# Optimization experiments

Measured on AMD Instinct MI355X. Metric: run time of the kernel, lower is better.

The kernel has to match this reference:

```python
import jax, jax.numpy as jnp
import numpy as np

E, S, D, A, L, H, C = 8, 6000, 128, 16, 64, 256, 64
B = 50            # no_batches hardcoded in torch forward
T = S // B        # number of outer integration steps
DT = 0.5          # solver dt; t_horizon=[0,1] -> 2 reversible-Heun substeps
NSUB = 2
SQDT = float(np.sqrt(DT))


def setup_inputs():
    ks = jax.random.split(jax.random.key(0), 24)
    w = lambda k, shp, s=0.05: (jax.random.normal(k, shp) * s).astype(jnp.float32)
    z = lambda shp: jnp.zeros(shp, jnp.float32)
    return dict(
        xs=w(ks[0], (E, S, D), 1.0),
        actions=w(ks[1], (E, S, A), 1.0),
        z0_noise=w(ks[2], (T, E, B, L), 1.0),
        dW=w(ks[3], (T, NSUB, E * B, L), 1.0),
        enc_w1=w(ks[4], (E, D, H)), enc_b1=z((E, H)),
        enc_w2=w(ks[5], (E, H, C)), enc_b2=z((E, C)),
        qz0_w=w(ks[6], (E, C, 2 * L)), qz0_b=z((E, 2 * L)),
        act_w=w(ks[7], (E, L + A + D, L)), act_b=z((E, L)),
        fw1=w(ks[8], (L, H)), fb1=z((H,)),
        fw2=w(ks[9], (H, H)), fb2=z((H,)),
        fw3=w(ks[10], (H, L)), fb3=z((L,)),
        hw1=w(ks[11], (L, H)), hb1=z((H,)),
        hw2=w(ks[12], (H, H)), hb2=z((H,)),
        hw3=w(ks[13], (H, L)), hb3=z((L,)),
        gw1=w(ks[14], (L, H)), gb1=z((L, H)),
        gw2=w(ks[15], (L, H), 0.02), gb2=jnp.ones((L,), jnp.float32),
        pw1=w(ks[16], (E, L, H)), pb1=z((E, H)),
        pw2=w(ks[17], (E, H, H)), pb2=z((E, H)),
        pw3=w(ks[18], (E, H, D)), pb3=z((E, D)),
        pz0_mean=z((E, 1, L)), pz0_logstd=z((E, 1, L)),
    )


def reference(xs, actions, z0_noise, dW,
              enc_w1, enc_b1, enc_w2, enc_b2, qz0_w, qz0_b, act_w, act_b,
              fw1, fb1, fw2, fb2, fw3, fb3, hw1, hb1, hw2, hb2, hw3, hb3,
              gw1, gb1, gw2, gb2, pw1, pb1, pw2, pb2, pw3, pb3,
              pz0_mean, pz0_logstd):
    xs_r = xs.reshape(E, T, B, D).transpose(1, 0, 2, 3)       # [T,E,B,D]
    act_r = actions.reshape(E, T, B, A).transpose(1, 0, 2, 3)  # [T,E,B,A]

    def mlp3(y, w1, b1, w2, b2, w3, b3):
        h1 = jax.nn.sigmoid(y @ w1 + b1)
        h2 = jax.nn.sigmoid(h1 @ w2 + b2)
        return h2 @ w3 + b3

    def g_fn(y):  # per-latent-dim diagonal diffusion nets, vectorized over L
        hc = jax.nn.sigmoid(y[..., None] * gw1 + gb1)          # [N,L,H]
        return jnp.sum(hc * gw2, axis=-1) + gb2                # [N,L]

    def drift_all(zc):
        fz = mlp3(zc, fw1, fb1, fw2, fb2, fw3, fb3)
        hz = mlp3(zc, hw1, hb1, hw2, hb2, hw3, hb3)
        gz = g_fn(zc)
        u = (fz - hz) / gz
        return fz, gz, 0.5 * jnp.sum(u * u, axis=-1)           # logqp drift

    def sde_solve(zini, dWs):  # reversible Heun, Stratonovich, logqp-augmented
        zc = zh = zini
        lc = lh = jnp.zeros(zini.shape[0], zini.dtype)
        fz, gz, lf = drift_all(zc)
        for k in range(NSUB):
            dWk = dWs[k] * SQDT
            zh_n = 2.0 * zc - zh + fz * DT + gz * dWk
            lh_n = 2.0 * lc - lh + lf * DT
            fz1, gz1, lf1 = drift_all(zh_n)
            zc = zc + 0.5 * (fz + fz1) * DT + 0.5 * (gz + gz1) * dWk
            lc = lc + 0.5 * (lf + lf1) * DT
            zh, lh, fz, gz, lf = zh_n, lh_n, fz1, gz1, lf1
        return zc, lc

    def step(z_prev, inp):
        i, x_i, a_i, n_i, dW_i = inp
        c1 = jax.nn.sigmoid(jnp.einsum('ebd,edh->ebh', x_i, enc_w1) + enc_b1[:, None])
        ctx = jnp.einsum('ebh,ehc->ebc', c1, enc_w2) + enc_b2[:, None]
        q = jnp.einsum('ebc,eck->ebk', ctx, qz0_w) + qz0_b[:, None]
        qm, ql = q[..., :L], q[..., L:]
        z0 = qm + jnp.exp(ql) * n_i
        z_in = jnp.where(i == 0, z0, z_prev)
        lat = jnp.concatenate([z_in, a_i, x_i], axis=-1)
        z_enc = jnp.einsum('ebf,efl->ebl', lat, act_w) + act_b[:, None]
        zf, lr = sde_solve(z_enc.reshape(E * B, L), dW_i)
        z_new = zf.reshape(E, B, L)
        p1 = jax.nn.sigmoid(jnp.einsum('ebl,elh->ebh', z_new, pw1) + pb1[:, None])
        p2 = jax.nn.sigmoid(jnp.einsum('ebh,ehk->ebk', p1, pw2) + pb2[:, None])
        xm = jnp.einsum('ebh,ehd->ebd', p2, pw3) + pb3[:, None]
        # KL(q(z0) || p(z0)) elementwise, p has mean pz0_mean, logstd pz0_logstd
        kl = (pz0_logstd - ql
              + (jnp.exp(2.0 * ql) + (qm - pz0_mean) ** 2) / (2.0 * jnp.exp(2.0 * pz0_logstd))
              - 0.5)
        logqp0 = kl.sum(-1).mean(-1)  # [E]
        return z_new, (xm, lr.reshape(E, B), logqp0)

    z_init = jnp.zeros((E, B, L), xs.dtype)
    _, (xm_all, lr_all, lq0_all) = jax.lax.scan(
        step, z_init, (jnp.arange(T), xs_r, act_r, z0_noise, dW))
    predicted_xs = xm_all.transpose(1, 0, 2, 3).reshape(E, T * B, D)
    logqp_path = lr_all.mean(-1).sum(0) + lq0_all.sum(0)  # [E]
    return logqp_path, predicted_xs
```

## Files before the change

kernel.cpp:

```cpp
#include <hip/hip_runtime.h>
#include <math.h>

#define E 8
#define S 6000
#define D 128
#define A 16
#define L 64
#define H 256
#define C 64
#define B 50
#define T 120
#define NSUB 2
#define FLAT 208
#define RTOT 400
#define RPB 10
#define NBLK (RTOT / RPB)
#define BGRP 10
#define NBG 5

#define DT 0.5f
#define SQDT 0.70710678118654752440f

#define GNT 4096
#define GYMIN (-128.0f)
#define GDY 0.0625f
#define GINVDY 16.0f

typedef __attribute__((ext_vector_type(8))) short bf16x8;
typedef __attribute__((ext_vector_type(4))) float f32x4;

#define MFMA16(a, b, c) __builtin_amdgcn_mfma_f32_16x16x32_bf16(a, b, c, 0, 0, 0)

__device__ __forceinline__ float sigf(float x) { return 1.0f / (1.0f + __expf(-x)); }

__device__ __forceinline__ unsigned short f2bf(float x) {
    union { float f; unsigned u; } v; v.f = x;
    unsigned r = (v.u + 0x7FFFu + ((v.u >> 16) & 1u)) >> 16;
    return (unsigned short)r;
}

__global__ void gtab_kernel(const float* __restrict__ gw1, const float* __restrict__ gb1,
                            const float* __restrict__ gw2, const float* __restrict__ gb2,
                            float* __restrict__ tab) {
    int idx = blockIdx.x * blockDim.x + threadIdx.x;
    if (idx >= L * GNT) return;
    int l = idx / GNT, i = idx % GNT;
    float y = GYMIN + (float)i * GDY;
    const float* w1 = gw1 + l * H;
    const float* b1 = gb1 + l * H;
    const float* w2 = gw2 + l * H;
    float acc = gb2[l];
    #pragma unroll 4
    for (int h = 0; h < H; ++h) acc += w2[h] * sigf(y * w1[h] + b1[h]);
    tab[idx] = acc;
}

__global__ void packB_kernel(const float* __restrict__ src, unsigned short* __restrict__ dst,
                             int K, int N) {
    int idx = blockIdx.x * 256 + threadIdx.x;
    if (idx >= K * N) return;
    int j = idx & 7;
    int lane = (idx >> 3) & 63;
    int t2 = idx >> 9;
    int KC = K >> 5;
    int kc = t2 % KC, n = t2 / KC;
    int k = (kc << 5) + ((lane >> 4) << 3) + j;
    int c = (n << 4) + (lane & 15);
    dst[idx] = f2bf(src[k * N + c]);
}

__global__ void packAW_kernel(const float* __restrict__ aw, unsigned short* __restrict__ dst) {
    int idx = blockIdx.x * 256 + threadIdx.x;
    if (idx >= E * L * L) return;
    int e = idx >> 12;
    int rem = idx & 4095;
    int j = rem & 7;
    int lane = (rem >> 3) & 63;
    int t2 = rem >> 9;
    int kc = t2 & 1, n = t2 >> 1;
    int k = (kc << 5) + ((lane >> 4) << 3) + j;
    int c = (n << 4) + (lane & 15);
    dst[idx] = f2bf(aw[((size_t)e * FLAT + k) * L + c]);
}

__global__ __launch_bounds__(256) void enc_kernel(const float* __restrict__ xs, const float* __restrict__ z0n,
                           const float* __restrict__ ew1, const float* __restrict__ eb1,
                           const float* __restrict__ ew2, const float* __restrict__ eb2,
                           const float* __restrict__ qw,  const float* __restrict__ qb,
                           const float* __restrict__ pm,  const float* __restrict__ pl,
                           float* __restrict__ z0buf, float* __restrict__ logqp0p) {
    int bid = blockIdx.x;
    int bg = bid % NBG; int te = bid / NBG; int e = te % E; int t = te / E;
    int tid = threadIdx.x;
    __shared__ float xsh[BGRP][D];
    __shared__ float c1s[BGRP][H];
    __shared__ float part[4][C][BGRP];
    __shared__ float ctxs[BGRP][C];
    __shared__ float qs[BGRP][2 * L];

    for (int i = tid; i < BGRP * D; i += 256) {
        int j = i / D, d = i % D;
        xsh[j][d] = xs[((size_t)e * S + (size_t)t * B + bg * BGRP + j) * D + d];
    }
    __syncthreads();
    {
        float bias = eb1[e * H + tid];
        float acc[BGRP];
        #pragma unroll
        for (int j = 0; j < BGRP; ++j) acc[j] = bias;
        const float* w = ew1 + (size_t)e * D * H + tid;
        #pragma unroll 4
        for (int d = 0; d < D; ++d) {
            float wv = w[(size_t)d * H];
            #pragma unroll
            for (int j = 0; j < BGRP; ++j) acc[j] += xsh[j][d] * wv;
        }
        #pragma unroll
        for (int j = 0; j < BGRP; ++j) c1s[j][tid] = sigf(acc[j]);
    }
    __syncthreads();
    {
        int c = tid & 63, kq = tid >> 6;
        float acc[BGRP];
        #pragma unroll
        for (int j = 0; j < BGRP; ++j) acc[j] = 0.f;
        const float* w = ew2 + (size_t)e * H * C + c;
        #pragma unroll 4
        for (int h = kq * 64; h < kq * 64 + 64; ++h) {
            float wv = w[(size_t)h * C];
            #pragma unroll
            for (int j = 0; j < BGRP; ++j) acc[j] += c1s[j][h] * wv;
        }
        #pragma unroll
        for (int j = 0; j < BGRP; ++j) part[kq][c][j] = acc[j];
    }
    __syncthreads();
    if (tid < C) {
        float bias = eb2[e * C + tid];
        #pragma unroll
        for (int j = 0; j < BGRP; ++j)
            ctxs[j][tid] = part[0][tid][j] + part[1][tid][j] + part[2][tid][j] + part[3][tid][j] + bias;
    }
    __syncthreads();
    if (tid < 2 * L) {
        float bias = qb[e * 2 * L + tid];
        float acc[BGRP];
        #pragma unroll
        for (int j = 0; j < BGRP; ++j) acc[j] = bias;
        const float* w = qw + (size_t)e * C * 2 * L + tid;
        #pragma unroll 4
        for (int c = 0; c < C; ++c) {
            float wv = w[(size_t)c * 2 * L];
            #pragma unroll
            for (int j = 0; j < BGRP; ++j) acc[j] += ctxs[j][c] * wv;
        }
        #pragma unroll
        for (int j = 0; j < BGRP; ++j) qs[j][tid] = acc[j];
    }
    __syncthreads();
    if (tid < L) {
        int l = tid;
        float kacc = 0.f;
        float m = pm[e * L + l], ls = pl[e * L + l];
        float inv2e = 1.0f / (2.0f * __expf(2.0f * ls));
        #pragma unroll
        for (int j = 0; j < BGRP; ++j) {
            float qm = qs[j][l], ql = qs[j][L + l];
            if (t == 0) {
                int b = bg * BGRP + j;
                float n = z0n[((size_t)e * B + b) * L + l];
                z0buf[((size_t)e * B + b) * L + l] = qm + __expf(ql) * n;
            }
            float dq = qm - m;
            kacc += ls - ql + (__expf(2.f * ql) + dq * dq) * inv2e - 0.5f;
        }
        #pragma unroll
        for (int off = 32; off; off >>= 1) kacc += __shfl_xor(kacc, off);
        if (l == 0) logqp0p[bid] = kacc / (float)B;
    }
}

__global__ __launch_bounds__(64) void ax_kernel(const float* __restrict__ xs, const float* __restrict__ actions,
                          const float* __restrict__ aw, const float* __restrict__ ab,
                          float* __restrict__ ax) {
    int bid = blockIdx.x;
    int bg = bid % NBG; int te = bid / NBG; int e = te % E; int t = te / E;
    int tid = threadIdx.x;
    __shared__ float xrow[BGRP][D];
    __shared__ float arow[BGRP][A];
    for (int i = tid; i < BGRP * D; i += 64) {
        int j = i / D, d = i % D;
        xrow[j][d] = xs[((size_t)e * S + (size_t)t * B + bg * BGRP + j) * D + d];
    }
    for (int i = tid; i < BGRP * A; i += 64) {
        int j = i / A, a = i % A;
        arow[j][a] = actions[((size_t)e * S + (size_t)t * B + bg * BGRP + j) * A + a];
    }
    __syncthreads();
    int l = tid;
    float acc[BGRP];
    float bias = ab[e * L + l];
    #pragma unroll
    for (int j = 0; j < BGRP; ++j) acc[j] = bias;
    const float* awp = aw + ((size_t)e * FLAT + L) * L + l;
    #pragma unroll 4
    for (int a = 0; a < A; ++a) {
        float wv = awp[(size_t)a * L];
        #pragma unroll
        for (int j = 0; j < BGRP; ++j) acc[j] += arow[j][a] * wv;
    }
    const float* xwp = aw + ((size_t)e * FLAT + L + A) * L + l;
    #pragma unroll 4
    for (int d = 0; d < D; ++d) {
        float wv = xwp[(size_t)d * L];
        #pragma unroll
        for (int j = 0; j < BGRP; ++j) acc[j] += xrow[j][d] * wv;
    }
    size_t rbase = (size_t)t * RTOT + e * B + bg * BGRP;
    #pragma unroll
    for (int j = 0; j < BGRP; ++j) ax[(rbase + j) * L + l] = acc[j];
}

__global__ __launch_bounds__(512, 2) void seq_kernel(
    const unsigned short* __restrict__ pkAW, const float* __restrict__ dW,
    const float* __restrict__ z0buf, const float* __restrict__ axbuf,
    const unsigned short* __restrict__ pk1, const unsigned short* __restrict__ pk2,
    const unsigned short* __restrict__ pk3,
    const float* __restrict__ fb1, const float* __restrict__ hb1,
    const float* __restrict__ fb2, const float* __restrict__ hb2,
    const float* __restrict__ fb3, const float* __restrict__ hb3,
    const float* __restrict__ gtab, float* __restrict__ z_all, float* __restrict__ rowlr)
{
    __shared__ __align__(16) bf16x8 w1L[4096];
    __shared__ __align__(16) unsigned short ybf[16 * 64];
    __shared__ __align__(16) unsigned short o1[2][16 * 256];
    __shared__ __align__(16) unsigned short o2[2][16 * 256];
    __shared__ float zcS[16][64], zhA[16][64], zhB[16][64];
    __shared__ float fzb[2][16][64], gzb[2][16][64];
    __shared__ float lfb[2][16], lcS[16], lrsum[16];

    int tid = threadIdx.x;
    int wv = tid >> 6;
    int lane = tid & 63;
    int rA = lane & 15, kg = lane >> 4;
    int r_base = blockIdx.x * RPB;
    int e = blockIdx.x / 5;
    int sw = (rA & 7) << 3;

    for (int i = tid; i < 4096; i += 512) w1L[i] = ((const bf16x8*)pk1)[i];

    int net = wv >> 2;
    int nt0 = (wv & 3) << 2;
    int n0 = wv & 3;
    bf16x8 W0r[2], W2r[32], W3r[8];
    {
        const bf16x8* p0 = (const bf16x8*)pkAW + (e << 9);
        #pragma unroll
        for (int kc = 0; kc < 2; ++kc) W0r[kc] = p0[(n0 * 2 + kc) * 64 + lane];
        const bf16x8* p2 = (const bf16x8*)pk2 + net * 8192;
        #pragma unroll
        for (int i2 = 0; i2 < 4; ++i2)
            #pragma unroll
            for (int kc = 0; kc < 8; ++kc)
                W2r[i2 * 8 + kc] = p2[((nt0 + i2) * 8 + kc) * 64 + lane];
        const bf16x8* p3 = (const bf16x8*)pk3 + net * 2048;
        #pragma unroll
        for (int kc = 0; kc < 8; ++kc) W3r[kc] = p3[(n0 * 8 + kc) * 64 + lane];
    }
    float biasA[4], biasB[4], biasC;
    {
        const float* b1 = net ? hb1 : fb1;
        const float* b2 = net ? hb2 : fb2;
        const float* b3 = net ? hb3 : fb3;
        #pragma unroll
        for (int i2 = 0; i2 < 4; ++i2) {
            biasA[i2] = b1[((nt0 + i2) << 4) + rA];
            biasB[i2] = b2[((nt0 + i2) << 4) + rA];
        }
        biasC = b3[(n0 << 4) + rA];
    }

    for (int i = tid; i < RPB * L; i += 512) {
        int r = i >> 6;
        ybf[i ^ ((r & 7) << 3)] = f2bf(z0buf[(size_t)r_base * L + i]);
    }
    if (tid < 16) lrsum[tid] = 0.f;
    __syncthreads();

    float* fhp = (float*)o1;

    auto drift = [&](const float (*__restrict__ ysrc)[64], int bo) {
        {
            bf16x8 A0 = *(const bf16x8*)&ybf[((rA << 6) + (kg << 3)) ^ sw];
            bf16x8 A1 = *(const bf16x8*)&ybf[((rA << 6) + 32 + (kg << 3)) ^ sw];
            f32x4 acc[4];
            #pragma unroll
            for (int i2 = 0; i2 < 4; ++i2) {
                acc[i2] = (f32x4){biasA[i2], biasA[i2], biasA[i2], biasA[i2]};
                acc[i2] = MFMA16(A0, w1L[net * 2048 + ((nt0 + i2) * 2 + 0) * 64 + lane], acc[i2]);
                acc[i2] = MFMA16(A1, w1L[net * 2048 + ((nt0 + i2) * 2 + 1) * 64 + lane], acc[i2]);
            }
            unsigned short* o1n = o1[net];
            #pragma unroll
            for (int i2 = 0; i2 < 4; ++i2) {
                int c = ((nt0 + i2) << 4) + rA;
                #pragma unroll
                for (int rr = 0; rr < 4; ++rr) {
                    int r = (kg << 2) + rr;
                    o1n[((r << 8) + c) ^ ((r & 7) << 3)] = f2bf(sigf(acc[i2][rr]));
                }
            }
        }
        __syncthreads();
        {
            const unsigned short* o1n = o1[net];
            f32x4 acc[4];
            #pragma unroll
            for (int i2 = 0; i2 < 4; ++i2)
                acc[i2] = (f32x4){biasB[i2], biasB[i2], biasB[i2], biasB[i2]};
            #pragma unroll
            for (int kc = 0; kc < 8; ++kc) {
                bf16x8 Ak = *(const bf16x8*)&o1n[((rA << 8) + (kc << 5) + (kg << 3)) ^ sw];
                #pragma unroll
                for (int i2 = 0; i2 < 4; ++i2)
                    acc[i2] = MFMA16(Ak, W2r[i2 * 8 + kc], acc[i2]);
            }
            unsigned short* o2n = o2[net];
            #pragma unroll
            for (int i2 = 0; i2 < 4; ++i2) {
                int c = ((nt0 + i2) << 4) + rA;
                #pragma unroll
                for (int rr = 0; rr < 4; ++rr) {
                    int r = (kg << 2) + rr;
                    o2n[((r << 8) + c) ^ ((r & 7) << 3)] = f2bf(sigf(acc[i2][rr]));
                }
            }
        }
        __syncthreads();
        {
            const unsigned short* o2n = o2[net];
            f32x4 acc = (f32x4){biasC, biasC, biasC, biasC};
            #pragma unroll
            for (int kc = 0; kc < 8; ++kc) {
                bf16x8 Ak = *(const bf16x8*)&o2n[((rA << 8) + (kc << 5) + (kg << 3)) ^ sw];
                acc = MFMA16(Ak, W3r[kc], acc);
            }
            int c = (n0 << 4) + rA;
            #pragma unroll
            for (int rr = 0; rr < 4; ++rr)
                fhp[net * 1024 + (((kg << 2) + rr) << 6) + c] = acc[rr];
        }
        __syncthreads();
        #pragma unroll
        for (int pass = 0; pass < 2; ++pass) {
            int r = wv + (pass << 3);
            if (r < RPB) {
                int l = lane;
                float fv = fhp[(r << 6) + l];
                float hv = fhp[1024 + (r << 6) + l];
                float yl = ysrc[r][l];
                float x = (yl - GYMIN) * GINVDY;
                x = fminf(fmaxf(x, 0.0f), (float)(GNT - 2) + 0.999f);
                int ii = (int)x;
                float fr = x - (float)ii;
                const float* tl = gtab + ((size_t)l << 12);
                float gv = tl[ii] * (1.0f - fr) + tl[ii + 1] * fr;
                float u = (fv - hv) / gv;
                fzb[bo][r][l] = fv;
                gzb[bo][r][l] = gv;
                float us = u * u;
                #pragma unroll
                for (int off = 32; off; off >>= 1) us += __shfl_xor(us, off);
                if (l == 0) lfb[bo][r] = 0.5f * us;
            }
        }
        __syncthreads();
    };

    for (int t = 0; t < T; ++t) {
        size_t axb = ((size_t)t * RTOT + r_base) * L;
        size_t db0 = ((size_t)(t * 2 + 0) * RTOT + r_base) * L;
        size_t db1 = ((size_t)(t * 2 + 1) * RTOT + r_base) * L;
        float ax0 = axbuf[axb + tid];
        float dwA0 = dW[db0 + tid] * SQDT;
        float dwB0 = dW[db1 + tid] * SQDT;
        float ax1 = 0.f, dwA1 = 0.f, dwB1 = 0.f;
        if (tid < RPB * L - 512) {
            ax1  = axbuf[axb + 512 + tid];
            dwA1 = dW[db0 + 512 + tid] * SQDT;
            dwB1 = dW[db1 + 512 + tid] * SQDT;
        }
        if (wv < 4) {
            bf16x8 Z0 = *(const bf16x8*)&ybf[((rA << 6) + (kg << 3)) ^ sw];
            bf16x8 Z1 = *(const bf16x8*)&ybf[((rA << 6) + 32 + (kg << 3)) ^ sw];
            f32x4 acc = (f32x4){0.f, 0.f, 0.f, 0.f};
            acc = MFMA16(Z0, W0r[0], acc);
            acc = MFMA16(Z1, W0r[1], acc);
            int c = (n0 << 4) + rA;
            #pragma unroll
            for (int rr = 0; rr < 4; ++rr)
                zcS[(kg << 2) + rr][c] = acc[rr];
        }
        if (tid < 16) lcS[tid] = 0.f;
        __syncthreads();
        {
            int r = tid >> 6, l = tid & 63;
            float v = zcS[r][l] + ax0;
            zcS[r][l] = v; zhA[r][l] = v;
            ybf[tid ^ ((r & 7) << 3)] = f2bf(v);
            if (tid < RPB * L - 512) {
                int i2 = tid + 512, r2 = i2 >> 6, l2 = i2 & 63;
                float v2 = zcS[r2][l2] + ax1;
                zcS[r2][l2] = v2; zhA[r2][l2] = v2;
                ybf[i2 ^ ((r2 & 7) << 3)] = f2bf(v2);
            }
        }
        __syncthreads();

        drift(zcS, 0);

        float (*zh)[64] = zhA;
        float (*zt)[64] = zhB;
        int cur = 0;
        #pragma unroll
        for (int k2 = 0; k2 < NSUB; ++k2) {
            int nxt = cur ^ 1;
            float dwv0 = k2 ? dwB0 : dwA0;
            float dwv1 = k2 ? dwB1 : dwA1;
            {
                int r = tid >> 6, l = tid & 63;
                float v = 2.f * zcS[r][l] - zh[r][l] + fzb[cur][r][l] * DT + gzb[cur][r][l] * dwv0;
                zt[r][l] = v;
                ybf[tid ^ ((r & 7) << 3)] = f2bf(v);
                if (tid < RPB * L - 512) {
                    int i2 = tid + 512, r2 = i2 >> 6, l2 = i2 & 63;
                    float v2 = 2.f * zcS[r2][l2] - zh[r2][l2] + fzb[cur][r2][l2] * DT + gzb[cur][r2][l2] * dwv1;
                    zt[r2][l2] = v2;
                    ybf[i2 ^ ((r2 & 7) << 3)] = f2bf(v2);
                }
            }
            __syncthreads();
            drift(zt, nxt);
            {
                int r = tid >> 6, l = tid & 63;
                zcS[r][l] += 0.5f * (fzb[cur][r][l] + fzb[nxt][r][l]) * DT
                           + 0.5f * (gzb[cur][r][l] + gzb[nxt][r][l]) * dwv0;
                if (tid < RPB * L - 512) {
                    int i2 = tid + 512, r2 = i2 >> 6, l2 = i2 & 63;
                    zcS[r2][l2] += 0.5f * (fzb[cur][r2][l2] + fzb[nxt][r2][l2]) * DT
                                 + 0.5f * (gzb[cur][r2][l2] + gzb[nxt][r2][l2]) * dwv1;
                }
            }
            if (tid < RPB) lcS[tid] += 0.5f * (lfb[cur][tid] + lfb[nxt][tid]) * DT;
            { float (*tmp)[64] = zh; zh = zt; zt = tmp; }
            cur = nxt;
            __syncthreads();
        }
        {
            int r = tid >> 6;
            float v = zcS[r][tid & 63];
            z_all[((size_t)t * RTOT + r_base) * L + tid] = v;
            ybf[tid ^ ((r & 7) << 3)] = f2bf(v);
            if (tid < RPB * L - 512) {
                int i2 = tid + 512, r2 = i2 >> 6;
                float v2 = zcS[r2][i2 & 63];
                z_all[((size_t)t * RTOT + r_base) * L + i2] = v2;
                ybf[i2 ^ ((r2 & 7) << 3)] = f2bf(v2);
            }
        }
        if (tid < RPB) lrsum[tid] += lcS[tid];
        __syncthreads();
    }
    if (tid < RPB) rowlr[r_base + tid] = lrsum[tid];
}

__global__ __launch_bounds__(256) void proj_kernel(const float* __restrict__ z_all,
                            const float* __restrict__ pw1, const float* __restrict__ pb1,
                            const float* __restrict__ pw2, const float* __restrict__ pb2,
                            const float* __restrict__ pw3, const float* __restrict__ pb3,
                            float* __restrict__ out) {
    int bid = blockIdx.x;
    int bg = bid % NBG; int te = bid / NBG; int e = te % E; int t = te / E;
    int tid = threadIdx.x;
    __shared__ float zs[BGRP][L];
    __shared__ float p1s[BGRP][H];
    __shared__ float p2s[BGRP][H];
    __shared__ float part3[D][BGRP];
    size_t rbase = (size_t)t * RTOT + e * B + bg * BGRP;
    for (int i = tid; i < BGRP * L; i += 256) {
        int j = i >> 6, ll = i & 63;
        zs[j][ll] = z_all[(rbase + j) * L + ll];
    }
    __syncthreads();
    {
        float bias = pb1[e * H + tid];
        float acc[BGRP];
        #pragma unroll
        for (int j = 0; j < BGRP; ++j) acc[j] = bias;
        const float* w = pw1 + (size_t)e * L * H + tid;
        #pragma unroll 4
        for (int k = 0; k < L; ++k) {
            float wv = w[(size_t)k * H];
            #pragma unroll
            for (int j = 0; j < BGRP; ++j) acc[j] += zs[j][k] * wv;
        }
        #pragma unroll
        for (int j = 0; j < BGRP; ++j) p1s[j][tid] = sigf(acc[j]);
    }
    __syncthreads();
    {
        float bias = pb2[e * H + tid];
        float acc[BGRP];
        #pragma unroll
        for (int j = 0; j < BGRP; ++j) acc[j] = bias;
        const float* w = pw2 + (size_t)e * H * H + tid;
        #pragma unroll 4
        for (int k = 0; k < H; ++k) {
            float wv = w[(size_t)k * H];
            #pragma unroll
            for (int j = 0; j < BGRP; ++j) acc[j] += p1s[j][k] * wv;
        }
        #pragma unroll
        for (int j = 0; j < BGRP; ++j) p2s[j][tid] = sigf(acc[j]);
    }
    __syncthreads();
    float acc3[BGRP];
    {
        int dd = tid & 127, kh = tid >> 7;
        #pragma unroll
        for (int j = 0; j < BGRP; ++j) acc3[j] = 0.f;
        const float* w = pw3 + (size_t)e * H * D + dd;
        #pragma unroll 4
        for (int k = kh * 128; k < kh * 128 + 128; ++k) {
            float wv = w[(size_t)k * D];
            #pragma unroll
            for (int j = 0; j < BGRP; ++j) acc3[j] += p2s[j][k] * wv;
        }
        if (kh == 1) {
            #pragma unroll
            for (int j = 0; j < BGRP; ++j) part3[dd][j] = acc3[j];
        }
    }
    __syncthreads();
    if (tid < D) {
        float bias = pb3[e * D + tid];
        #pragma unroll
        for (int j = 0; j < BGRP; ++j) {
            out[8 + ((size_t)e * S + (size_t)t * B + bg * BGRP + j) * D + tid]
                = acc3[j] + part3[tid][j] + bias;
        }
    }
}

__global__ void fin_kernel(const float* __restrict__ logqp0p, const float* __restrict__ rowlr,
                           float* __restrict__ out) {
    int e = threadIdx.x;
    if (e < E) {
        float acc = 0.f;
        for (int t = 0; t < T; ++t)
            for (int bg = 0; bg < NBG; ++bg)
                acc += logqp0p[(t * E + e) * NBG + bg];
        float s = 0.f;
        for (int b = 0; b < B; ++b) s += rowlr[e * B + b];
        out[e] = acc + s / (float)B;
    }
}

extern "C" void kernel_launch(void* const* d_in, const int* in_sizes, int n_in,
                              void* d_out, int out_size, void* d_ws, size_t ws_size,
                              hipStream_t stream) {
    const float* xs      = (const float*)d_in[0];
    const float* actions = (const float*)d_in[1];
    const float* z0n     = (const float*)d_in[2];
    const float* dWp     = (const float*)d_in[3];
    const float* ew1     = (const float*)d_in[4];
    const float* eb1     = (const float*)d_in[5];
    const float* ew2     = (const float*)d_in[6];
    const float* eb2     = (const float*)d_in[7];
    const float* qw      = (const float*)d_in[8];
    const float* qb      = (const float*)d_in[9];
    const float* aw      = (const float*)d_in[10];
    const float* ab      = (const float*)d_in[11];
    const float* fw1     = (const float*)d_in[12];
    const float* fb1     = (const float*)d_in[13];
    const float* fw2     = (const float*)d_in[14];
    const float* fb2     = (const float*)d_in[15];
    const float* fw3     = (const float*)d_in[16];
    const float* fb3     = (const float*)d_in[17];
    const float* hw1     = (const float*)d_in[18];
    const float* hb1     = (const float*)d_in[19];
    const float* hw2     = (const float*)d_in[20];
    const float* hb2     = (const float*)d_in[21];
    const float* hw3     = (const float*)d_in[22];
    const float* hb3     = (const float*)d_in[23];
    const float* gw1     = (const float*)d_in[24];
    const float* gb1     = (const float*)d_in[25];
    const float* gw2     = (const float*)d_in[26];
    const float* gb2     = (const float*)d_in[27];
    const float* pw1     = (const float*)d_in[28];
    const float* pb1     = (const float*)d_in[29];
    const float* pw2     = (const float*)d_in[30];
    const float* pb2     = (const float*)d_in[31];
    const float* pw3     = (const float*)d_in[32];
    const float* pb3     = (const float*)d_in[33];
    const float* pm      = (const float*)d_in[34];
    const float* pl      = (const float*)d_in[35];

    float* ws      = (float*)d_ws;
    float* z0buf   = ws;
    float* axbuf   = z0buf + 25600;
    float* z_all   = axbuf + 3072000;
    float* logqp0p = z_all + 3072000;
    float* rowlr   = logqp0p + 4800;
    float* gtab    = rowlr + 400;
    unsigned short* pku = (unsigned short*)(gtab + 262144);
    unsigned short* pk1 = pku;
    unsigned short* pk2 = pk1 + 32768;
    unsigned short* pk3 = pk2 + 131072;
    unsigned short* pkAW = pk3 + 32768;
    float* out     = (float*)d_out;

    packB_kernel<<<64,  256, 0, stream>>>(fw1, pk1,          64, 256);
    packB_kernel<<<64,  256, 0, stream>>>(hw1, pk1 + 16384,  64, 256);
    packB_kernel<<<256, 256, 0, stream>>>(fw2, pk2,          256, 256);
    packB_kernel<<<256, 256, 0, stream>>>(hw2, pk2 + 65536,  256, 256);
    packB_kernel<<<64,  256, 0, stream>>>(fw3, pk3,          256, 64);
    packB_kernel<<<64,  256, 0, stream>>>(hw3, pk3 + 16384,  256, 64);
    packAW_kernel<<<128, 256, 0, stream>>>(aw, pkAW);
    gtab_kernel<<<1024, 256, 0, stream>>>(gw1, gb1, gw2, gb2, gtab);
    enc_kernel<<<T * E * NBG, 256, 0, stream>>>(xs, z0n, ew1, eb1, ew2, eb2, qw, qb, pm, pl, z0buf, logqp0p);
    ax_kernel<<<T * E * NBG, 64, 0, stream>>>(xs, actions, aw, ab, axbuf);
    seq_kernel<<<NBLK, 512, 0, stream>>>(pkAW, dWp, z0buf, axbuf,
                                         pk1, pk2, pk3,
                                         fb1, hb1, fb2, hb2, fb3, hb3,
                                         gtab, z_all, rowlr);
    proj_kernel<<<T * E * NBG, 256, 0, stream>>>(z_all, pw1, pb1, pw2, pb2, pw3, pb3, out);
    fin_kernel<<<1, 64, 0, stream>>>(logqp0p, rowlr, out);
}
```

Before: 3.155 ms.

## Double seq_kernel threads to 1024 and split MLP work across more waves

The sequential SDE kernel now launches 1024 threads per block instead of 512. Each wave handles half as many output tiles in layers 1 and 2, and layer 3 is split along K into two halves whose partial sums are added through shared memory. The diffusion-table lookup is also moved earlier, into the z-update phase, so its global loads overlap the MLP. The aim is to shorten the serial critical path of each step. The cost is more waves contending at every barrier and an extra shared-memory reduction.

```diff
diff --git a/kernel.cpp b/kernel.cpp
--- a/kernel.cpp
+++ b/kernel.cpp
@@ -221,7 +221,7 @@
     for (int j = 0; j < BGRP; ++j) ax[(rbase + j) * L + l] = acc[j];
 }
 
-__global__ __launch_bounds__(512, 2) void seq_kernel(
+__global__ __launch_bounds__(1024, 4) void seq_kernel(
     const unsigned short* __restrict__ pkAW, const float* __restrict__ dW,
     const float* __restrict__ z0buf, const float* __restrict__ axbuf,
     const unsigned short* __restrict__ pk1, const unsigned short* __restrict__ pk2,
@@ -235,75 +235,89 @@
     __shared__ __align__(16) unsigned short ybf[16 * 64];
     __shared__ __align__(16) unsigned short o1[2][16 * 256];
     __shared__ __align__(16) unsigned short o2[2][16 * 256];
+    __shared__ float fh2[2][2][RPB][64];
     __shared__ float zcS[16][64], zhA[16][64], zhB[16][64];
-    __shared__ float fzb[2][16][64], gzb[2][16][64];
-    __shared__ float lfb[2][16], lcS[16], lrsum[16];
+    __shared__ float fzb[2][RPB][64], gzb[2][RPB][64];
+    __shared__ float lfb[2][RPB], lcS[RPB], lrsum[RPB];
 
     int tid = threadIdx.x;
     int wv = tid >> 6;
     int lane = tid & 63;
     int rA = lane & 15, kg = lane >> 4;
+    int sw = (rA & 7) << 3;
     int r_base = blockIdx.x * RPB;
     int e = blockIdx.x / 5;
-    int sw = (rA & 7) << 3;
-
-    for (int i = tid; i < 4096; i += 512) w1L[i] = ((const bf16x8*)pk1)[i];
-
-    int net = wv >> 2;
-    int nt0 = (wv & 3) << 2;
+
+    for (int i = tid; i < 4096; i += 1024) w1L[i] = ((const bf16x8*)pk1)[i];
+
+    int net = wv >> 3;
+    int na = (wv & 7) << 1;
+    int cnet = wv >> 3, crem = wv & 7, n0c = crem >> 1, kh = crem & 1;
     int n0 = wv & 3;
-    bf16x8 W0r[2], W2r[32], W3r[8];
+
+    bf16x8 W0r[2], W2r[16], W3r[4];
     {
         const bf16x8* p0 = (const bf16x8*)pkAW + (e << 9);
-        #pragma unroll
-        for (int kc = 0; kc < 2; ++kc) W0r[kc] = p0[(n0 * 2 + kc) * 64 + lane];
+        W0r[0] = p0[(n0 * 2 + 0) * 64 + lane];
+        W0r[1] = p0[(n0 * 2 + 1) * 64 + lane];
         const bf16x8* p2 = (const bf16x8*)pk2 + net * 8192;
         #pragma unroll
-        for (int i2 = 0; i2 < 4; ++i2)
+        for (int i2 = 0; i2 < 2; ++i2)
             #pragma unroll
             for (int kc = 0; kc < 8; ++kc)
-                W2r[i2 * 8 + kc] = p2[((nt0 + i2) * 8 + kc) * 64 + lane];
-        const bf16x8* p3 = (const bf16x8*)pk3 + net * 2048;
-        #pragma unroll
-        for (int kc = 0; kc < 8; ++kc) W3r[kc] = p3[(n0 * 8 + kc) * 64 + lane];
-    }
-    float biasA[4], biasB[4], biasC;
+                W2r[i2 * 8 + kc] = p2[((na + i2) * 8 + kc) * 64 + lane];
+        const bf16x8* p3 = (const bf16x8*)pk3 + cnet * 2048;
+        #pragma unroll
+        for (int kc = 0; kc < 4; ++kc)
+            W3r[kc] = p3[(n0c * 8 + kh * 4 + kc) * 64 + lane];
+    }
+    float biasA[2], biasB[2], biasC;
     {
         const float* b1 = net ? hb1 : fb1;
         const float* b2 = net ? hb2 : fb2;
-        const float* b3 = net ? hb3 : fb3;
-        #pragma unroll
-        for (int i2 = 0; i2 < 4; ++i2) {
-            biasA[i2] = b1[((nt0 + i2) << 4) + rA];
-            biasB[i2] = b2[((nt0 + i2) << 4) + rA];
-        }
-        biasC = b3[(n0 << 4) + rA];
-    }
-
-    for (int i = tid; i < RPB * L; i += 512) {
+        const float* b3 = cnet ? hb3 : fb3;
+        biasA[0] = b1[((na + 0) << 4) + rA];
+        biasA[1] = b1[((na + 1) << 4) + rA];
+        biasB[0] = b2[((na + 0) << 4) + rA];
+        biasB[1] = b2[((na + 1) << 4) + rA];
+        biasC = kh ? 0.f : b3[(n0c << 4) + rA];
+    }
+
+    for (int i = tid; i < 16 * 64; i += 1024) {
         int r = i >> 6;
-        ybf[i ^ ((r & 7) << 3)] = f2bf(z0buf[(size_t)r_base * L + i]);
-    }
-    if (tid < 16) lrsum[tid] = 0.f;
-    __syncthreads();
-
-    float* fhp = (float*)o1;
-
-    auto drift = [&](const float (*__restrict__ ysrc)[64], int bo) {
+        float v = (i < RPB * L) ? z0buf[(size_t)r_base * L + i] : 0.f;
+        ybf[i ^ ((r & 7) << 3)] = f2bf(v);
+    }
+    if (tid < RPB) lrsum[tid] = 0.f;
+    __syncthreads();
+
+    float gt0 = 1.f, gt1 = 1.f, gfr = 0.f;
+
+    auto gprep = [&](float v, int l) {
+        float x = (v - GYMIN) * GINVDY;
+        x = fminf(fmaxf(x, 0.0f), (float)(GNT - 2) + 0.999f);
+        int ii = (int)x;
+        gfr = x - (float)ii;
+        const float* tl = gtab + ((size_t)l << 12);
+        gt0 = tl[ii];
+        gt1 = tl[ii + 1];
+    };
+
+    auto drift = [&](int bo) {
         {
             bf16x8 A0 = *(const bf16x8*)&ybf[((rA << 6) + (kg << 3)) ^ sw];
             bf16x8 A1 = *(const bf16x8*)&ybf[((rA << 6) + 32 + (kg << 3)) ^ sw];
-            f32x4 acc[4];
-            #pragma unroll
-            for (int i2 = 0; i2 < 4; ++i2) {
+            f32x4 acc[2];
+            #pragma unroll
+            for (int i2 = 0; i2 < 2; ++i2) {
                 acc[i2] = (f32x4){biasA[i2], biasA[i2], biasA[i2], biasA[i2]};
-                acc[i2] = MFMA16(A0, w1L[net * 2048 + ((nt0 + i2) * 2 + 0) * 64 + lane], acc[i2]);
-                acc[i2] = MFMA16(A1, w1L[net * 2048 + ((nt0 + i2) * 2 + 1) * 64 + lane], acc[i2]);
+                acc[i2] = MFMA16(A0, w1L[net * 2048 + ((na + i2) * 2 + 0) * 64 + lane], acc[i2]);
+                acc[i2] = MFMA16(A1, w1L[net * 2048 + ((na + i2) * 2 + 1) * 64 + lane], acc[i2]);
             }
             unsigned short* o1n = o1[net];
             #pragma unroll
-            for (int i2 = 0; i2 < 4; ++i2) {
-                int c = ((nt0 + i2) << 4) + rA;
+            for (int i2 = 0; i2 < 2; ++i2) {
+                int c = ((na + i2) << 4) + rA;
                 #pragma unroll
                 for (int rr = 0; rr < 4; ++rr) {
                     int r = (kg << 2) + rr;
@@ -314,81 +328,63 @@
         __syncthreads();
         {
             const unsigned short* o1n = o1[net];
-            f32x4 acc[4];
-            #pragma unroll
-            for (int i2 = 0; i2 < 4; ++i2)
-                acc[i2] = (f32x4){biasB[i2], biasB[i2], biasB[i2], biasB[i2]};
+            f32x4 acc0 = (f32x4){biasB[0], biasB[0], biasB[0], biasB[0]};
+            f32x4 acc1 = (f32x4){biasB[1], biasB[1], biasB[1], biasB[1]};
             #pragma unroll
             for (int kc = 0; kc < 8; ++kc) {
                 bf16x8 Ak = *(const bf16x8*)&o1n[((rA << 8) + (kc << 5) + (kg << 3)) ^ sw];
-                #pragma unroll
-                for (int i2 = 0; i2 < 4; ++i2)
-                    acc[i2] = MFMA16(Ak, W2r[i2 * 8 + kc], acc[i2]);
+                acc0 = MFMA16(Ak, W2r[kc], acc0);
+                acc1 = MFMA16(Ak, W2r[8 + kc], acc1);
             }
             unsigned short* o2n = o2[net];
             #pragma unroll
-            for (int i2 = 0; i2 < 4; ++i2) {
-                int c = ((nt0 + i2) << 4) + rA;
-                #pragma unroll
-                for (int rr = 0; rr < 4; ++rr) {
-                    int r = (kg << 2) + rr;
-                    o2n[((r << 8) + c) ^ ((r & 7) << 3)] = f2bf(sigf(acc[i2][rr]));
-                }
+            for (int rr = 0; rr < 4; ++rr) {
+                int r = (kg << 2) + rr;
+                int c0 = ((na + 0) << 4) + rA;
+                int c1 = ((na + 1) << 4) + rA;
+                o2n[((r << 8) + c0) ^ ((r & 7) << 3)] = f2bf(sigf(acc0[rr]));
+                o2n[((r << 8) + c1) ^ ((r & 7) << 3)] = f2bf(sigf(acc1[rr]));
             }
         }
         __syncthreads();
         {
-            const unsigned short* o2n = o2[net];
+            const unsigned short* o2n = o2[cnet];
             f32x4 acc = (f32x4){biasC, biasC, biasC, biasC};
             #pragma unroll
-            for (int kc = 0; kc < 8; ++kc) {
-                bf16x8 Ak = *(const bf16x8*)&o2n[((rA << 8) + (kc << 5) + (kg << 3)) ^ sw];
+            for (int kc = 0; kc < 4; ++kc) {
+                bf16x8 Ak = *(const bf16x8*)&o2n[((rA << 8) + (((kh << 2) + kc) << 5) + (kg << 3)) ^ sw];
                 acc = MFMA16(Ak, W3r[kc], acc);
             }
-            int c = (n0 << 4) + rA;
-            #pragma unroll
-            for (int rr = 0; rr < 4; ++rr)
-                fhp[net * 1024 + (((kg << 2) + rr) << 6) + c] = acc[rr];
+            int c = (n0c << 4) + rA;
+            #pragma unroll
+            for (int rr = 0; rr < 4; ++rr) {
+                int r = (kg << 2) + rr;
+                if (r < RPB) fh2[cnet][kh][r][c] = acc[rr];
+            }
         }
         __syncthreads();
-        #pragma unroll
-        for (int pass = 0; pass < 2; ++pass) {
-            int r = wv + (pass << 3);
-            if (r < RPB) {
-                int l = lane;
-                float fv = fhp[(r << 6) + l];
-                float hv = fhp[1024 + (r << 6) + l];
-                float yl = ysrc[r][l];
-                float x = (yl - GYMIN) * GINVDY;
-                x = fminf(fmaxf(x, 0.0f), (float)(GNT - 2) + 0.999f);
-                int ii = (int)x;
-                float fr = x - (float)ii;
-                const float* tl = gtab + ((size_t)l << 12);
-                float gv = tl[ii] * (1.0f - fr) + tl[ii + 1] * fr;
-                float u = (fv - hv) / gv;
-                fzb[bo][r][l] = fv;
-                gzb[bo][r][l] = gv;
-                float us = u * u;
-                #pragma unroll
-                for (int off = 32; off; off >>= 1) us += __shfl_xor(us, off);
-                if (l == 0) lfb[bo][r] = 0.5f * us;
-            }
+        if (wv < RPB) {
+            int r = wv, l = lane;
+            float fv = fh2[0][0][r][l] + fh2[0][1][r][l];
+            float hv = fh2[1][0][r][l] + fh2[1][1][r][l];
+            float gv = gt0 * (1.0f - gfr) + gt1 * gfr;
+            float u = (fv - hv) / gv;
+            fzb[bo][r][l] = fv;
+            gzb[bo][r][l] = gv;
+            float us = u * u;
+            #pragma unroll
+            for (int off = 32; off; off >>= 1) us += __shfl_xor(us, off);
+            if (l == 0) lfb[bo][r] = 0.5f * us;
         }
         __syncthreads();
     };
 
     for (int t = 0; t < T; ++t) {
-        size_t axb = ((size_t)t * RTOT + r_base) * L;
-        size_t db0 = ((size_t)(t * 2 + 0) * RTOT + r_base) * L;
-        size_t db1 = ((size_t)(t * 2 + 1) * RTOT + r_base) * L;
-        float ax0 = axbuf[axb + tid];
-        float dwA0 = dW[db0 + tid] * SQDT;
-        float dwB0 = dW[db1 + tid] * SQDT;
-        float ax1 = 0.f, dwA1 = 0.f, dwB1 = 0.f;
-        if (tid < RPB * L - 512) {
-            ax1  = axbuf[axb + 512 + tid];
-            dwA1 = dW[db0 + 512 + tid] * SQDT;
-            dwB1 = dW[db1 + 512 + tid] * SQDT;
+        float ax0 = 0.f, dwA0 = 0.f, dwB0 = 0.f;
+        if (tid < RPB * L) {
+            ax0  = axbuf[((size_t)t * RTOT + r_base) * L + tid];
+            dwA0 = dW[((size_t)(t * 2 + 0) * RTOT + r_base) * L + tid] * SQDT;
+            dwB0 = dW[((size_t)(t * 2 + 1) * RTOT + r_base) * L + tid] * SQDT;
         }
         if (wv < 4) {
             bf16x8 Z0 = *(const bf16x8*)&ybf[((rA << 6) + (kg << 3)) ^ sw];
@@ -401,23 +397,18 @@
             for (int rr = 0; rr < 4; ++rr)
                 zcS[(kg << 2) + rr][c] = acc[rr];
         }
-        if (tid < 16) lcS[tid] = 0.f;
+        if (tid < RPB) lcS[tid] = 0.f;
         __syncthreads();
-        {
+        if (tid < RPB * L) {
             int r = tid >> 6, l = tid & 63;
             float v = zcS[r][l] + ax0;
             zcS[r][l] = v; zhA[r][l] = v;
             ybf[tid ^ ((r & 7) << 3)] = f2bf(v);
-            if (tid < RPB * L - 512) {
-                int i2 = tid + 512, r2 = i2 >> 6, l2 = i2 & 63;
-                float v2 = zcS[r2][l2] + ax1;
-                zcS[r2][l2] = v2; zhA[r2][l2] = v2;
-                ybf[i2 ^ ((r2 & 7) << 3)] = f2bf(v2);
-            }
+            gprep(v, l);
         }
         __syncthreads();
 
-        drift(zcS, 0);
+        drift(0);
 
         float (*zh)[64] = zhA;
         float (*zt)[64] = zhB;
@@ -425,48 +416,31 @@
         #pragma unroll
         for (int k2 = 0; k2 < NSUB; ++k2) {
             int nxt = cur ^ 1;
-            float dwv0 = k2 ? dwB0 : dwA0;
-            float dwv1 = k2 ? dwB1 : dwA1;
-            {
+            float dwv = k2 ? dwB0 : dwA0;
+            if (tid < RPB * L) {
                 int r = tid >> 6, l = tid & 63;
-                float v = 2.f * zcS[r][l] - zh[r][l] + fzb[cur][r][l] * DT + gzb[cur][r][l] * dwv0;
+                float v = 2.f * zcS[r][l] - zh[r][l] + fzb[cur][r][l] * DT + gzb[cur][r][l] * dwv;
                 zt[r][l] = v;
                 ybf[tid ^ ((r & 7) << 3)] = f2bf(v);
-                if (tid < RPB * L - 512) {
-                    int i2 = tid + 512, r2 = i2 >> 6, l2 = i2 & 63;
-                    float v2 = 2.f * zcS[r2][l2] - zh[r2][l2] + fzb[cur][r2][l2] * DT + gzb[cur][r2][l2] * dwv1;
-                    zt[r2][l2] = v2;
-                    ybf[i2 ^ ((r2 & 7) << 3)] = f2bf(v2);
-                }
+                gprep(v, l);
             }
             __syncthreads();
-            drift(zt, nxt);
-            {
+            drift(nxt);
+            if (tid < RPB * L) {
                 int r = tid >> 6, l = tid & 63;
                 zcS[r][l] += 0.5f * (fzb[cur][r][l] + fzb[nxt][r][l]) * DT
-                           + 0.5f * (gzb[cur][r][l] + gzb[nxt][r][l]) * dwv0;
-                if (tid < RPB * L - 512) {
-                    int i2 = tid + 512, r2 = i2 >> 6, l2 = i2 & 63;
-                    zcS[r2][l2] += 0.5f * (fzb[cur][r2][l2] + fzb[nxt][r2][l2]) * DT
-                                 + 0.5f * (gzb[cur][r2][l2] + gzb[nxt][r2][l2]) * dwv1;
-                }
+                           + 0.5f * (gzb[cur][r][l] + gzb[nxt][r][l]) * dwv;
             }
             if (tid < RPB) lcS[tid] += 0.5f * (lfb[cur][tid] + lfb[nxt][tid]) * DT;
             { float (*tmp)[64] = zh; zh = zt; zt = tmp; }
             cur = nxt;
             __syncthreads();
         }
-        {
+        if (tid < RPB * L) {
             int r = tid >> 6;
             float v = zcS[r][tid & 63];
             z_all[((size_t)t * RTOT + r_base) * L + tid] = v;
             ybf[tid ^ ((r & 7) << 3)] = f2bf(v);
-            if (tid < RPB * L - 512) {
-                int i2 = tid + 512, r2 = i2 >> 6;
-                float v2 = zcS[r2][i2 & 63];
-                z_all[((size_t)t * RTOT + r_base) * L + i2] = v2;
-                ybf[i2 ^ ((r2 & 7) << 3)] = f2bf(v2);
-            }
         }
         if (tid < RPB) lrsum[tid] += lcS[tid];
         __syncthreads();
@@ -630,10 +604,10 @@
     gtab_kernel<<<1024, 256, 0, stream>>>(gw1, gb1, gw2, gb2, gtab);
     enc_kernel<<<T * E * NBG, 256, 0, stream>>>(xs, z0n, ew1, eb1, ew2, eb2, qw, qb, pm, pl, z0buf, logqp0p);
     ax_kernel<<<T * E * NBG, 64, 0, stream>>>(xs, actions, aw, ab, axbuf);
-    seq_kernel<<<NBLK, 512, 0, stream>>>(pkAW, dWp, z0buf, axbuf,
-                                         pk1, pk2, pk3,
-                                         fb1, hb1, fb2, hb2, fb3, hb3,
-                                         gtab, z_all, rowlr);
+    seq_kernel<<<NBLK, 1024, 0, stream>>>(pkAW, dWp, z0buf, axbuf,
+                                          pk1, pk2, pk3,
+                                          fb1, hb1, fb2, hb2, fb3, hb3,
+                                          gtab, z_all, rowlr);
     proj_kernel<<<T * E * NBG, 256, 0, stream>>>(z_all, pw1, pb1, pw2, pb2, pw3, pb3, out);
     fin_kernel<<<1, 64, 0, stream>>>(logqp0p, rowlr, out);
 }
```

After: 3.314 ms. 5.1% more time.
